# Performance work log

Hardware: AMD Instinct MI355X
Metric: run time of the kernel (lower is better)

## Reference

```python
import jax, jax.numpy as jnp
import numpy as np

N = 50000
E = 800000
D_IN, D_HID, D_OUT = 128, 128, 64


def setup_inputs() -> dict:
    key = jax.random.key(0)
    ks = jax.random.split(key, 8)
    x = jax.random.normal(ks[0], (N, D_IN), dtype=jnp.float32)
    edge_index = jax.random.randint(ks[1], (2, E), 0, N, dtype=jnp.int64)
    # Glorot-ish init for weights
    W1 = jax.random.normal(ks[2], (D_IN, D_HID), dtype=jnp.float32) / np.sqrt(D_IN)
    b1 = jnp.zeros((D_HID,), dtype=jnp.float32)
    W2 = jax.random.normal(ks[3], (D_HID, D_OUT), dtype=jnp.float32) / np.sqrt(D_HID)
    b2 = jnp.zeros((D_OUT,), dtype=jnp.float32)
    fc_W = jax.random.normal(ks[4], (D_OUT, D_OUT), dtype=jnp.float32) / np.sqrt(D_OUT)
    fc_b = jnp.zeros((D_OUT,), dtype=jnp.float32)
    return {"x": x, "edge_index": edge_index, "W1": W1, "b1": b1,
            "W2": W2, "b2": b2, "fc_W": fc_W, "fc_b": fc_b}


def _gcn_norm(edge_index, n_nodes):
    # PyG GCNConv default: add self-loops, symmetric normalization
    src, dst = edge_index[0], edge_index[1]
    loops = jnp.arange(n_nodes, dtype=edge_index.dtype)
    src = jnp.concatenate([src, loops])
    dst = jnp.concatenate([dst, loops])
    deg = jax.ops.segment_sum(jnp.ones_like(dst, dtype=jnp.float32), dst,
                              num_segments=n_nodes)
    dinv = jnp.where(deg > 0, jax.lax.rsqrt(deg), 0.0)
    norm = dinv[src] * dinv[dst]  # [E + N]
    return src, dst, norm


def _gcn_conv(x, src, dst, norm, W, b):
    h = x @ W                          # [N, d_out] transform first (fewer FLOPs)
    msg = h[src] * norm[:, None]       # gather + scale  [E+N, d_out]
    out = jax.ops.segment_sum(msg, dst, num_segments=x.shape[0])
    return out + b


def reference(x, edge_index, W1, b1, W2, b2, fc_W, fc_b):
    src, dst, norm = _gcn_norm(edge_index, x.shape[0])
    h = jax.nn.relu(_gcn_conv(x, src, dst, norm, W1, b1))
    h = jax.nn.relu(_gcn_conv(h, src, dst, norm, W2, b2))
    return h @ fc_W + fc_b
```

## Files before the change

kernel.cpp:

```cpp
#include <hip/hip_runtime.h>
#include <hip/hip_bf16.h>


typedef __attribute__((ext_vector_type(8))) short bf16x8;
typedef __attribute__((ext_vector_type(4))) float f32x4;

#define SLAB 64
#define BCAP 6144
#define BINCH 8192

__device__ __forceinline__ unsigned short f2bf(float f) {
    unsigned u = __float_as_uint(f);
    unsigned r = (u + 0x7FFFu + ((u >> 16) & 1u)) >> 16;
    return (unsigned short)r;
}
__device__ __forceinline__ float bf16_lo(unsigned u) {
    return __uint_as_float((u & 0xFFFFu) << 16);
}
__device__ __forceinline__ float bf16_hi(unsigned u) {
    return __uint_as_float(u & 0xFFFF0000u);
}


__global__ void k_wt(const float* __restrict__ W1, const float* __restrict__ W2,
                     const float* __restrict__ fcW,
                     unsigned short* __restrict__ W1T, unsigned short* __restrict__ W2T,
                     unsigned short* __restrict__ fcWT, int* __restrict__ gcnt,
                     unsigned short* __restrict__ hs1r, unsigned short* __restrict__ hs2,
                     float* __restrict__ dinv, int n) {
    int j = blockIdx.x * blockDim.x + threadIdx.x;
    if (j < 256) gcnt[j] = 0;
    if (j < 16384) {
        int m = j >> 7, k = j & 127;
        W1T[j] = f2bf(W1[k * 128 + m]);
    } else if (j < 24576) {
        int q = j - 16384;
        int m = q >> 7, k = q & 127;
        W2T[q] = f2bf(W2[k * 64 + m]);
    } else if (j < 28672) {
        int q = j - 24576;
        int m = q >> 6, k = q & 63;
        fcWT[q] = f2bf(fcW[k * 64 + m]);
    } else if (j < 28800) {
        hs1r[(size_t)n * 128 + (j - 28672)] = 0;
    } else if (j < 28864) {
        hs2[(size_t)n * 64 + (j - 28800)] = 0;
    } else if (j == 28864) {
        dinv[n] = 0.0f;
    }
}


__device__ __forceinline__ void gemm1_body(const float* __restrict__ X,
                                           const unsigned short* __restrict__ W1T,
                                           unsigned short* __restrict__ outp,
                                           int n, int blk, int tid,
                                           unsigned short* xs) {
    constexpr int LDW = 136;
    int base = blk * 64;
    for (int idx = tid; idx < 64 * 32; idx += 256) {
        int r = idx >> 5, c = idx & 31;
        int row = base + r;
        float4 v = make_float4(0.f, 0.f, 0.f, 0.f);
        if (row < n) v = ((const float4*)X)[(size_t)row * 32 + c];
        unsigned short* dp = &xs[r * LDW + c * 4];
        dp[0] = f2bf(v.x); dp[1] = f2bf(v.y); dp[2] = f2bf(v.z); dp[3] = f2bf(v.w);
    }
    __syncthreads();

    int wave = tid >> 6, lane = tid & 63;
    int quad = lane >> 4, l16 = lane & 15;
    int rbase = wave * 16;

    bf16x8 af[4];
#pragma unroll
    for (int kb = 0; kb < 4; ++kb)
        af[kb] = *(const bf16x8*)&xs[(rbase + l16) * LDW + kb * 32 + quad * 8];

#pragma unroll
    for (int jt = 0; jt < 8; ++jt) {
        f32x4 acc = {0.f, 0.f, 0.f, 0.f};
#pragma unroll
        for (int kb = 0; kb < 4; ++kb) {
            bf16x8 bf = *(const bf16x8*)&W1T[(size_t)(jt * 16 + l16) * 128 + kb * 32 + quad * 8];
            acc = __builtin_amdgcn_mfma_f32_16x16x32_bf16(af[kb], bf, acc, 0, 0, 0);
        }
#pragma unroll
        for (int r = 0; r < 4; ++r) {
            int row = base + rbase + quad * 4 + r;
            if (row < n)
                outp[(size_t)row * 128 + jt * 16 + l16] = f2bf(acc[r]);
        }
    }
}


__global__ __launch_bounds__(1024) void k_front(
    const int* __restrict__ src, const int* __restrict__ dst, int e,
    int* __restrict__ gcnt, unsigned* __restrict__ staging,
    const float* __restrict__ x, const unsigned short* __restrict__ W1T,
    unsigned short* __restrict__ hs1r, int n, int nbk, int ngemm) {
    __shared__ __align__(16) unsigned short xs4[4][64 * 136];
    __shared__ int bcnt[256], bpos[256], gofs[256];
    int bid = (int)blockIdx.x, tid = (int)threadIdx.x;

    if (bid < ngemm) {
        int tile = tid >> 8;
        gemm1_body(x, W1T, hs1r, n, bid * 4 + tile, tid & 255, xs4[tile]);
    } else {
        int b0 = bid - ngemm;
        if (tid < 256) { bcnt[tid] = 0; bpos[tid] = 0; }
        __syncthreads();
        int e0 = b0 * BINCH;
        int d[8], s[8];
#pragma unroll
        for (int r = 0; r < 8; ++r) {
            int i = e0 + r * 1024 + tid;
            if (i < e) { d[r] = dst[i]; s[r] = src[i]; } else d[r] = -1;
        }
#pragma unroll
        for (int r = 0; r < 8; ++r)
            if (d[r] >= 0) atomicAdd(&bcnt[d[r] >> 8], 1);
        __syncthreads();
        if (tid < nbk) {
            int c = bcnt[tid];
            gofs[tid] = c ? atomicAdd(&gcnt[tid], c) : 0;
        }
        __syncthreads();
#pragma unroll
        for (int r = 0; r < 8; ++r) {
            if (d[r] >= 0) {
                int b = d[r] >> 8;
                int p = atomicAdd(&bpos[b], 1);
                int idx = gofs[b] + p;
                if (idx < BCAP)
                    staging[(size_t)b * BCAP + idx] =
                        ((unsigned)d[r] << 16) | (unsigned)s[r];
            }
        }
    }
}


__global__ __launch_bounds__(1024) void k_scatter(
    const unsigned* __restrict__ staging, const int* __restrict__ gcnt,
    int* __restrict__ cnt, unsigned short* __restrict__ col,
    float* __restrict__ dinv, int n) {
    __shared__ int lcnt[256];
    __shared__ __align__(16) unsigned short ls[256 * SLAB];
    int b = (int)blockIdx.x, t = (int)threadIdx.x;
    if (t < 256) lcnt[t] = 0;
    unsigned sent2 = (unsigned)n | ((unsigned)n << 16);
    for (int i = t; i < 256 * SLAB / 2; i += 1024) ((unsigned*)ls)[i] = sent2;
    __syncthreads();
    int eb = gcnt[b]; if (eb > BCAP) eb = BCAP;
    const unsigned* sp = staging + (size_t)b * BCAP;
    for (int i = t; i < eb; i += 1024) {
        unsigned pk = sp[i];
        int dl = (int)(pk >> 16) & 255;
        int pos = atomicAdd(&lcnt[dl], 1);
        if (pos < SLAB) ls[(dl << 6) + pos] = (unsigned short)(pk & 0xFFFFu);
    }
    __syncthreads();
    int base = b << 8;
    const uint4* lsv = (const uint4*)ls;
    uint4* gv = (uint4*)(col + ((size_t)base << 6));
    for (int i = t; i < 256 * SLAB / 8; i += 1024) gv[i] = lsv[i];
    if (t < 256 && base + t < n) {
        int c = lcnt[t];
        cnt[base + t] = c;
        dinv[base + t] = rsqrtf((float)c + 1.0f);
    }
}


__global__ __launch_bounds__(256) void k_aggg128(
    const int* __restrict__ cnt, const unsigned short* __restrict__ col,
    const unsigned short* __restrict__ hs, const float* __restrict__ dinv,
    const float* __restrict__ bias, const unsigned short* __restrict__ W2T,
    unsigned short* __restrict__ hs2, int n) {
    __shared__ __align__(16) unsigned short ys[16 * 136];
    __shared__ float ldi[16];
    int tid = (int)threadIdx.x;
    int w = tid >> 6, lane = tid & 63;
    int half = lane >> 5, l32 = lane & 31;
    int gbase = (int)blockIdx.x * 16;
    const uint2* hp2 = (const uint2*)hs;

    for (int p = 0; p < 2; ++p) {
        int lrow = w * 4 + p * 2;
        int nodeA = gbase + lrow;
        int node = nodeA + half;
        int dA = cnt[nodeA], dB = cnt[nodeA + 1];
        if (dA > SLAB) dA = SLAB;
        if (dB > SLAB) dB = SLAB;
        int dmax = dA > dB ? dA : dB;
        const unsigned short* cp = &col[(size_t)node * SLAB];
        float di = dinv[node];
        uint2 su = hp2[(size_t)node * 32 + l32];
        float a0 = di * bf16_lo(su.x), a1 = di * bf16_hi(su.x);
        float a2 = di * bf16_lo(su.y), a3 = di * bf16_hi(su.y);
        float c0a = 0.f, c1a = 0.f, c2a = 0.f, c3a = 0.f;

        for (int i = 0; i < dmax; i += 16) {
            uint4 cA = *(const uint4*)&cp[i];
            uint4 cB = *(const uint4*)&cp[i + 8];
            int ci[16];
            ci[0] = cA.x & 0xFFFF; ci[1] = cA.x >> 16;
            ci[2] = cA.y & 0xFFFF; ci[3] = cA.y >> 16;
            ci[4] = cA.z & 0xFFFF; ci[5] = cA.z >> 16;
            ci[6] = cA.w & 0xFFFF; ci[7] = cA.w >> 16;
            ci[8] = cB.x & 0xFFFF; ci[9] = cB.x >> 16;
            ci[10] = cB.y & 0xFFFF; ci[11] = cB.y >> 16;
            ci[12] = cB.z & 0xFFFF; ci[13] = cB.z >> 16;
            ci[14] = cB.w & 0xFFFF; ci[15] = cB.w >> 16;
            uint2 u[16];
#pragma unroll
            for (int j = 0; j < 16; ++j) u[j] = hp2[(size_t)ci[j] * 32 + l32];
            float dw[16];
#pragma unroll
            for (int j = 0; j < 16; ++j) dw[j] = dinv[ci[j]];
#pragma unroll
            for (int j = 0; j < 16; j += 2) {
                a0 = fmaf(dw[j], bf16_lo(u[j].x), a0);
                a1 = fmaf(dw[j], bf16_hi(u[j].x), a1);
                a2 = fmaf(dw[j], bf16_lo(u[j].y), a2);
                a3 = fmaf(dw[j], bf16_hi(u[j].y), a3);
                c0a = fmaf(dw[j + 1], bf16_lo(u[j + 1].x), c0a);
                c1a = fmaf(dw[j + 1], bf16_hi(u[j + 1].x), c1a);
                c2a = fmaf(dw[j + 1], bf16_lo(u[j + 1].y), c2a);
                c3a = fmaf(dw[j + 1], bf16_hi(u[j + 1].y), c3a);
            }
        }
        float r0 = a0 + c0a, r1 = a1 + c1a, r2 = a2 + c2a, r3 = a3 + c3a;
        float4 bv = *(const float4*)&bias[l32 * 4];
        float v0 = fmaxf(di * r0 + bv.x, 0.0f);
        float v1 = fmaxf(di * r1 + bv.y, 0.0f);
        float v2 = fmaxf(di * r2 + bv.z, 0.0f);
        float v3 = fmaxf(di * r3 + bv.w, 0.0f);
        unsigned o0 = (unsigned)f2bf(v0) | ((unsigned)f2bf(v1) << 16);
        unsigned o1 = (unsigned)f2bf(v2) | ((unsigned)f2bf(v3) << 16);
        *(uint2*)((char*)ys + (size_t)(lrow + half) * 272 + l32 * 8) = make_uint2(o0, o1);
        if (l32 == 0) ldi[lrow + half] = di;
    }
    __syncthreads();

    int quad = lane >> 4, l16 = lane & 15;
    bf16x8 a[4];
#pragma unroll
    for (int kb = 0; kb < 4; ++kb)
        a[kb] = *(const bf16x8*)&ys[l16 * 136 + kb * 32 + quad * 8];
    f32x4 acc = {0.f, 0.f, 0.f, 0.f};
#pragma unroll
    for (int kb = 0; kb < 4; ++kb) {
        bf16x8 bf = *(const bf16x8*)&W2T[(size_t)(w * 16 + l16) * 128 + kb * 32 + quad * 8];
        acc = __builtin_amdgcn_mfma_f32_16x16x32_bf16(a[kb], bf, acc, 0, 0, 0);
    }
#pragma unroll
    for (int r = 0; r < 4; ++r) {
        int lrow = quad * 4 + r;
        int row = gbase + lrow;
        if (row < n)
            hs2[(size_t)row * 64 + w * 16 + l16] = f2bf(acc[r] * ldi[lrow]);
    }
}


__global__ __launch_bounds__(256) void k_aggg64(
    const int* __restrict__ cnt, const unsigned short* __restrict__ col,
    const unsigned short* __restrict__ hs, const float* __restrict__ dinv,
    const float* __restrict__ bias, const unsigned short* __restrict__ fcWT,
    const float* __restrict__ fcb, float* __restrict__ out, int n) {
    __shared__ __align__(16) unsigned short yt[16 * 72];
    int tid = (int)threadIdx.x;
    int w = tid >> 6, lane = tid & 63;
    int half = lane >> 5, l32 = lane & 31;
    int gbase = (int)blockIdx.x * 16;
    const unsigned* hp = (const unsigned*)hs;

    for (int p = 0; p < 2; ++p) {
        int lrow = w * 4 + p * 2;
        int nodeA = gbase + lrow;
        int node = nodeA + half;
        int dA = cnt[nodeA], dB = cnt[nodeA + 1];
        if (dA > SLAB) dA = SLAB;
        if (dB > SLAB) dB = SLAB;
        int dmax = dA > dB ? dA : dB;
        const unsigned short* cp = &col[(size_t)node * SLAB];
        float di = dinv[node];
        unsigned su = hp[(size_t)node * 32 + l32];
        float a0 = bf16_lo(su), a1 = bf16_hi(su);
        float b0 = 0.f, b1 = 0.f;

        for (int i = 0; i < dmax; i += 16) {
            uint4 cA = *(const uint4*)&cp[i];
            uint4 cB = *(const uint4*)&cp[i + 8];
            int ci[16];
            ci[0] = cA.x & 0xFFFF; ci[1] = cA.x >> 16;
            ci[2] = cA.y & 0xFFFF; ci[3] = cA.y >> 16;
            ci[4] = cA.z & 0xFFFF; ci[5] = cA.z >> 16;
            ci[6] = cA.w & 0xFFFF; ci[7] = cA.w >> 16;
            ci[8] = cB.x & 0xFFFF; ci[9] = cB.x >> 16;
            ci[10] = cB.y & 0xFFFF; ci[11] = cB.y >> 16;
            ci[12] = cB.z & 0xFFFF; ci[13] = cB.z >> 16;
            ci[14] = cB.w & 0xFFFF; ci[15] = cB.w >> 16;
            unsigned u[16];
#pragma unroll
            for (int j = 0; j < 16; ++j) u[j] = hp[(size_t)ci[j] * 32 + l32];
#pragma unroll
            for (int j = 0; j < 16; j += 2) {
                a0 += bf16_lo(u[j]);     a1 += bf16_hi(u[j]);
                b0 += bf16_lo(u[j + 1]); b1 += bf16_hi(u[j + 1]);
            }
        }
        float2 bv = *(const float2*)&bias[l32 * 2];
        float v0 = fmaxf(di * (a0 + b0) + bv.x, 0.0f);
        float v1 = fmaxf(di * (a1 + b1) + bv.y, 0.0f);
        *(unsigned*)((char*)yt + (size_t)(lrow + half) * 144 + l32 * 4) =
            (unsigned)f2bf(v0) | ((unsigned)f2bf(v1) << 16);
    }
    __syncthreads();

    int quad = lane >> 4, l16 = lane & 15;
    bf16x8 a[2];
#pragma unroll
    for (int kb = 0; kb < 2; ++kb)
        a[kb] = *(const bf16x8*)&yt[l16 * 72 + kb * 32 + quad * 8];
    f32x4 acc = {0.f, 0.f, 0.f, 0.f};
#pragma unroll
    for (int kb = 0; kb < 2; ++kb) {
        bf16x8 bf = *(const bf16x8*)&fcWT[(size_t)(w * 16 + l16) * 64 + kb * 32 + quad * 8];
        acc = __builtin_amdgcn_mfma_f32_16x16x32_bf16(a[kb], bf, acc, 0, 0, 0);
    }
    float bv = fcb[w * 16 + l16];
#pragma unroll
    for (int r = 0; r < 4; ++r) {
        int row = gbase + quad * 4 + r;
        if (row < n)
            out[(size_t)row * 64 + w * 16 + l16] = acc[r] + bv;
    }
}


extern "C" void kernel_launch(void* const* d_in, const int* in_sizes, int n_in,
                              void* d_out, int out_size, void* d_ws, size_t ws_size,
                              hipStream_t stream) {
    const float* x   = (const float*)d_in[0];
    const int*   ei  = (const int*)d_in[1];
    const float* W1  = (const float*)d_in[2];
    const float* b1  = (const float*)d_in[3];
    const float* W2  = (const float*)d_in[4];
    const float* b2  = (const float*)d_in[5];
    const float* fcW = (const float*)d_in[6];
    const float* fcb = (const float*)d_in[7];
    float* out = (float*)d_out;

    const int N = in_sizes[0] / 128;
    const int E = in_sizes[1] / 2;
    const int* src = ei;
    const int* dst = ei + E;

    const int NB    = (N + 255) >> 8;
    const int Npad  = NB << 8;
    const int nbin  = (E + BINCH - 1) / BINCH;
    const int gg64  = (N + 63) / 64;
    const int ngemm = (gg64 + 3) / 4;
    const int nagg  = (N + 15) / 16;

    auto align16 = [](size_t v) { return (v + 15) & ~(size_t)15; };
    char* p = (char*)d_ws;
    int* gcnt = (int*)p;                       p += align16(sizeof(int) * 256);
    unsigned* staging = (unsigned*)p;          p += align16(sizeof(unsigned) * (size_t)NB * BCAP);
    int* cnt = (int*)p;                        p += align16(sizeof(int) * N);
    float* dinv = (float*)p;                   p += align16(sizeof(float) * (N + 1));
    unsigned short* col = (unsigned short*)p;  p += align16(sizeof(unsigned short) * (size_t)Npad * SLAB);
    unsigned short* W1T = (unsigned short*)p;  p += align16(2 * 128 * 128);
    unsigned short* W2T = (unsigned short*)p;  p += align16(2 * 64 * 128);
    unsigned short* fcWT = (unsigned short*)p; p += align16(2 * 64 * 64);
    unsigned short* hs1r = (unsigned short*)p; p += align16(2 * ((size_t)N + 1) * 128);
    unsigned short* hs2 = (unsigned short*)p;  p += align16(2 * ((size_t)N + 1) * 64);

    k_wt<<<114, 256, 0, stream>>>(W1, W2, fcW, W1T, W2T, fcWT, gcnt,
                                  hs1r, hs2, dinv, N);

    k_front<<<ngemm + nbin, 1024, 0, stream>>>(src, dst, E, gcnt, staging,
                                               x, W1T, hs1r, N, NB, ngemm);
    k_scatter<<<NB, 1024, 0, stream>>>(staging, gcnt, cnt, col, dinv, N);

    k_aggg128<<<nagg, 256, 0, stream>>>(cnt, col, hs1r, dinv, b1, W2T, hs2, N);

    k_aggg64<<<nagg, 256, 0, stream>>>(cnt, col, hs2, dinv, b2, fcWT, fcb, out, N);
}
```

Before: 183.8 us.

## Prescale layer-1 features by dinv in scatter and process two nodes per wave

The scatter kernel now multiplies each node's layer-1 transformed features by its dinv in place, so the first aggregation no longer gathers dinv per neighbor and just sums pre-scaled rows. Both aggregation kernels are restructured so each half-wave handles two nodes at once with interleaved gathers, exposing more memory-level parallelism. The extra pass rewrites hs1 in place, costing additional read and write traffic and an extra bf16 rounding. cnt and dinv are padded to Npad so out-of-range nodes can be read safely.

```diff
diff --git a/kernel.cpp b/kernel.cpp
--- a/kernel.cpp
+++ b/kernel.cpp
@@ -20,6 +20,16 @@
 __device__ __forceinline__ float bf16_hi(unsigned u) {
     return __uint_as_float(u & 0xFFFF0000u);
 }
+
+#define UNPK16(cA, cB, ci)                                        \
+    ci[0] = cA.x & 0xFFFFu;  ci[1] = cA.x >> 16;                  \
+    ci[2] = cA.y & 0xFFFFu;  ci[3] = cA.y >> 16;                  \
+    ci[4] = cA.z & 0xFFFFu;  ci[5] = cA.z >> 16;                  \
+    ci[6] = cA.w & 0xFFFFu;  ci[7] = cA.w >> 16;                  \
+    ci[8] = cB.x & 0xFFFFu;  ci[9] = cB.x >> 16;                  \
+    ci[10] = cB.y & 0xFFFFu; ci[11] = cB.y >> 16;                 \
+    ci[12] = cB.z & 0xFFFFu; ci[13] = cB.z >> 16;                 \
+    ci[14] = cB.w & 0xFFFFu; ci[15] = cB.w >> 16;
 
 
 __global__ void k_wt(const float* __restrict__ W1, const float* __restrict__ W2,
@@ -27,7 +37,7 @@
                      unsigned short* __restrict__ W1T, unsigned short* __restrict__ W2T,
                      unsigned short* __restrict__ fcWT, int* __restrict__ gcnt,
                      unsigned short* __restrict__ hs1r, unsigned short* __restrict__ hs2,
-                     float* __restrict__ dinv, int n) {
+                     int n) {
     int j = blockIdx.x * blockDim.x + threadIdx.x;
     if (j < 256) gcnt[j] = 0;
     if (j < 16384) {
@@ -45,8 +55,6 @@
         hs1r[(size_t)n * 128 + (j - 28672)] = 0;
     } else if (j < 28864) {
         hs2[(size_t)n * 64 + (j - 28800)] = 0;
-    } else if (j == 28864) {
-        dinv[n] = 0.0f;
     }
 }
 
@@ -145,9 +153,10 @@
 __global__ __launch_bounds__(1024) void k_scatter(
     const unsigned* __restrict__ staging, const int* __restrict__ gcnt,
     int* __restrict__ cnt, unsigned short* __restrict__ col,
-    float* __restrict__ dinv, int n) {
+    float* __restrict__ dinv, unsigned* __restrict__ hs1u, int n) {
     __shared__ int lcnt[256];
     __shared__ __align__(16) unsigned short ls[256 * SLAB];
+    __shared__ float sdi[256];
     int b = (int)blockIdx.x, t = (int)threadIdx.x;
     if (t < 256) lcnt[t] = 0;
     unsigned sent2 = (unsigned)n | ((unsigned)n << 16);
@@ -166,10 +175,23 @@
     const uint4* lsv = (const uint4*)ls;
     uint4* gv = (uint4*)(col + ((size_t)base << 6));
     for (int i = t; i < 256 * SLAB / 8; i += 1024) gv[i] = lsv[i];
-    if (t < 256 && base + t < n) {
+    if (t < 256) {
         int c = lcnt[t];
+        float dv = rsqrtf((float)c + 1.0f);
+        sdi[t] = dv;
         cnt[base + t] = c;
-        dinv[base + t] = rsqrtf((float)c + 1.0f);
+        dinv[base + t] = dv;
+    }
+    __syncthreads();
+    int rows = n - base; if (rows > 256) rows = 256; if (rows < 0) rows = 0;
+    unsigned* hp = hs1u + ((size_t)base << 6);
+    for (int i = t; i < rows * 64; i += 1024) {
+        int r = i >> 6;
+        unsigned u = hp[i];
+        float sc = sdi[r];
+        unsigned lo = f2bf(sc * bf16_lo(u));
+        unsigned hi = f2bf(sc * bf16_hi(u));
+        hp[i] = lo | (hi << 16);
     }
 }
 
@@ -187,62 +209,65 @@
     int gbase = (int)blockIdx.x * 16;
     const uint2* hp2 = (const uint2*)hs;
 
-    for (int p = 0; p < 2; ++p) {
-        int lrow = w * 4 + p * 2;
-        int nodeA = gbase + lrow;
-        int node = nodeA + half;
-        int dA = cnt[nodeA], dB = cnt[nodeA + 1];
-        if (dA > SLAB) dA = SLAB;
-        if (dB > SLAB) dB = SLAB;
-        int dmax = dA > dB ? dA : dB;
-        const unsigned short* cp = &col[(size_t)node * SLAB];
-        float di = dinv[node];
-        uint2 su = hp2[(size_t)node * 32 + l32];
-        float a0 = di * bf16_lo(su.x), a1 = di * bf16_hi(su.x);
-        float a2 = di * bf16_lo(su.y), a3 = di * bf16_hi(su.y);
-        float c0a = 0.f, c1a = 0.f, c2a = 0.f, c3a = 0.f;
-
-        for (int i = 0; i < dmax; i += 16) {
-            uint4 cA = *(const uint4*)&cp[i];
-            uint4 cB = *(const uint4*)&cp[i + 8];
-            int ci[16];
-            ci[0] = cA.x & 0xFFFF; ci[1] = cA.x >> 16;
-            ci[2] = cA.y & 0xFFFF; ci[3] = cA.y >> 16;
-            ci[4] = cA.z & 0xFFFF; ci[5] = cA.z >> 16;
-            ci[6] = cA.w & 0xFFFF; ci[7] = cA.w >> 16;
-            ci[8] = cB.x & 0xFFFF; ci[9] = cB.x >> 16;
-            ci[10] = cB.y & 0xFFFF; ci[11] = cB.y >> 16;
-            ci[12] = cB.z & 0xFFFF; ci[13] = cB.z >> 16;
-            ci[14] = cB.w & 0xFFFF; ci[15] = cB.w >> 16;
-            uint2 u[16];
-#pragma unroll
-            for (int j = 0; j < 16; ++j) u[j] = hp2[(size_t)ci[j] * 32 + l32];
-            float dw[16];
-#pragma unroll
-            for (int j = 0; j < 16; ++j) dw[j] = dinv[ci[j]];
-#pragma unroll
-            for (int j = 0; j < 16; j += 2) {
-                a0 = fmaf(dw[j], bf16_lo(u[j].x), a0);
-                a1 = fmaf(dw[j], bf16_hi(u[j].x), a1);
-                a2 = fmaf(dw[j], bf16_lo(u[j].y), a2);
-                a3 = fmaf(dw[j], bf16_hi(u[j].y), a3);
-                c0a = fmaf(dw[j + 1], bf16_lo(u[j + 1].x), c0a);
-                c1a = fmaf(dw[j + 1], bf16_hi(u[j + 1].x), c1a);
-                c2a = fmaf(dw[j + 1], bf16_lo(u[j + 1].y), c2a);
-                c3a = fmaf(dw[j + 1], bf16_hi(u[j + 1].y), c3a);
-            }
-        }
-        float r0 = a0 + c0a, r1 = a1 + c1a, r2 = a2 + c2a, r3 = a3 + c3a;
-        float4 bv = *(const float4*)&bias[l32 * 4];
-        float v0 = fmaxf(di * r0 + bv.x, 0.0f);
-        float v1 = fmaxf(di * r1 + bv.y, 0.0f);
-        float v2 = fmaxf(di * r2 + bv.z, 0.0f);
-        float v3 = fmaxf(di * r3 + bv.w, 0.0f);
+    int n0 = gbase + w * 4 + half;
+    int n1 = n0 + 2;
+    int c0 = cnt[n0]; if (c0 > SLAB) c0 = SLAB;
+    int c1 = cnt[n1]; if (c1 > SLAB) c1 = SLAB;
+    int dm = c0 > c1 ? c0 : c1;
+    int dmo = __shfl_xor(dm, 32);
+    if (dmo > dm) dm = dmo;
+
+    const unsigned short* cp0 = &col[(size_t)n0 * SLAB];
+    const unsigned short* cp1 = &col[(size_t)n1 * SLAB];
+    float di0 = dinv[n0], di1 = dinv[n1];
+    int h0 = n0 < n ? n0 : n, h1 = n1 < n ? n1 : n;
+    uint2 s0 = hp2[(size_t)h0 * 32 + l32];
+    uint2 s1 = hp2[(size_t)h1 * 32 + l32];
+    float a0 = bf16_lo(s0.x), a1 = bf16_hi(s0.x), a2 = bf16_lo(s0.y), a3 = bf16_hi(s0.y);
+    float b0 = bf16_lo(s1.x), b1 = bf16_hi(s1.x), b2 = bf16_lo(s1.y), b3 = bf16_hi(s1.y);
+
+    for (int i = 0; i < dm; i += 16) {
+        uint4 cA0 = *(const uint4*)&cp0[i];
+        uint4 cB0 = *(const uint4*)&cp0[i + 8];
+        uint4 cA1 = *(const uint4*)&cp1[i];
+        uint4 cB1 = *(const uint4*)&cp1[i + 8];
+        unsigned ci0[16], ci1[16];
+        UNPK16(cA0, cB0, ci0)
+        UNPK16(cA1, cB1, ci1)
+        uint2 u0[16], u1[16];
+#pragma unroll
+        for (int j = 0; j < 16; ++j) u0[j] = hp2[(size_t)ci0[j] * 32 + l32];
+#pragma unroll
+        for (int j = 0; j < 16; ++j) u1[j] = hp2[(size_t)ci1[j] * 32 + l32];
+#pragma unroll
+        for (int j = 0; j < 16; ++j) {
+            a0 += bf16_lo(u0[j].x); a1 += bf16_hi(u0[j].x);
+            a2 += bf16_lo(u0[j].y); a3 += bf16_hi(u0[j].y);
+            b0 += bf16_lo(u1[j].x); b1 += bf16_hi(u1[j].x);
+            b2 += bf16_lo(u1[j].y); b3 += bf16_hi(u1[j].y);
+        }
+    }
+
+    float4 bv = *(const float4*)&bias[l32 * 4];
+    {
+        float v0 = fmaxf(di0 * a0 + bv.x, 0.0f);
+        float v1 = fmaxf(di0 * a1 + bv.y, 0.0f);
+        float v2 = fmaxf(di0 * a2 + bv.z, 0.0f);
+        float v3 = fmaxf(di0 * a3 + bv.w, 0.0f);
         unsigned o0 = (unsigned)f2bf(v0) | ((unsigned)f2bf(v1) << 16);
         unsigned o1 = (unsigned)f2bf(v2) | ((unsigned)f2bf(v3) << 16);
-        *(uint2*)((char*)ys + (size_t)(lrow + half) * 272 + l32 * 8) = make_uint2(o0, o1);
-        if (l32 == 0) ldi[lrow + half] = di;
-    }
+        *(uint2*)((char*)ys + (size_t)(w * 4 + half) * 272 + l32 * 8) = make_uint2(o0, o1);
+    }
+    {
+        float v0 = fmaxf(di1 * b0 + bv.x, 0.0f);
+        float v1 = fmaxf(di1 * b1 + bv.y, 0.0f);
+        float v2 = fmaxf(di1 * b2 + bv.z, 0.0f);
+        float v3 = fmaxf(di1 * b3 + bv.w, 0.0f);
+        unsigned o0 = (unsigned)f2bf(v0) | ((unsigned)f2bf(v1) << 16);
+        unsigned o1 = (unsigned)f2bf(v2) | ((unsigned)f2bf(v3) << 16);
+        *(uint2*)((char*)ys + (size_t)(w * 4 + 2 + half) * 272 + l32 * 8) = make_uint2(o0, o1);
+    }
+    if (l32 == 0) { ldi[w * 4 + half] = di0; ldi[w * 4 + 2 + half] = di1; }
     __syncthreads();
 
     int quad = lane >> 4, l16 = lane & 15;
@@ -278,45 +303,54 @@
     int gbase = (int)blockIdx.x * 16;
     const unsigned* hp = (const unsigned*)hs;
 
-    for (int p = 0; p < 2; ++p) {
-        int lrow = w * 4 + p * 2;
-        int nodeA = gbase + lrow;
-        int node = nodeA + half;
-        int dA = cnt[nodeA], dB = cnt[nodeA + 1];
-        if (dA > SLAB) dA = SLAB;
-        if (dB > SLAB) dB = SLAB;
-        int dmax = dA > dB ? dA : dB;
-        const unsigned short* cp = &col[(size_t)node * SLAB];
-        float di = dinv[node];
-        unsigned su = hp[(size_t)node * 32 + l32];
-        float a0 = bf16_lo(su), a1 = bf16_hi(su);
-        float b0 = 0.f, b1 = 0.f;
-
-        for (int i = 0; i < dmax; i += 16) {
-            uint4 cA = *(const uint4*)&cp[i];
-            uint4 cB = *(const uint4*)&cp[i + 8];
-            int ci[16];
-            ci[0] = cA.x & 0xFFFF; ci[1] = cA.x >> 16;
-            ci[2] = cA.y & 0xFFFF; ci[3] = cA.y >> 16;
-            ci[4] = cA.z & 0xFFFF; ci[5] = cA.z >> 16;
-            ci[6] = cA.w & 0xFFFF; ci[7] = cA.w >> 16;
-            ci[8] = cB.x & 0xFFFF; ci[9] = cB.x >> 16;
-            ci[10] = cB.y & 0xFFFF; ci[11] = cB.y >> 16;
-            ci[12] = cB.z & 0xFFFF; ci[13] = cB.z >> 16;
-            ci[14] = cB.w & 0xFFFF; ci[15] = cB.w >> 16;
-            unsigned u[16];
-#pragma unroll
-            for (int j = 0; j < 16; ++j) u[j] = hp[(size_t)ci[j] * 32 + l32];
-#pragma unroll
-            for (int j = 0; j < 16; j += 2) {
-                a0 += bf16_lo(u[j]);     a1 += bf16_hi(u[j]);
-                b0 += bf16_lo(u[j + 1]); b1 += bf16_hi(u[j + 1]);
-            }
-        }
-        float2 bv = *(const float2*)&bias[l32 * 2];
-        float v0 = fmaxf(di * (a0 + b0) + bv.x, 0.0f);
-        float v1 = fmaxf(di * (a1 + b1) + bv.y, 0.0f);
-        *(unsigned*)((char*)yt + (size_t)(lrow + half) * 144 + l32 * 4) =
+    int n0 = gbase + w * 4 + half;
+    int n1 = n0 + 2;
+    int c0 = cnt[n0]; if (c0 > SLAB) c0 = SLAB;
+    int c1 = cnt[n1]; if (c1 > SLAB) c1 = SLAB;
+    int dm = c0 > c1 ? c0 : c1;
+    int dmo = __shfl_xor(dm, 32);
+    if (dmo > dm) dm = dmo;
+
+    const unsigned short* cp0 = &col[(size_t)n0 * SLAB];
+    const unsigned short* cp1 = &col[(size_t)n1 * SLAB];
+    float di0 = dinv[n0], di1 = dinv[n1];
+    int h0 = n0 < n ? n0 : n, h1 = n1 < n ? n1 : n;
+    unsigned s0 = hp[(size_t)h0 * 32 + l32];
+    unsigned s1 = hp[(size_t)h1 * 32 + l32];
+    float a0 = bf16_lo(s0), a1 = bf16_hi(s0);
+    float b0 = bf16_lo(s1), b1 = bf16_hi(s1);
+
+    for (int i = 0; i < dm; i += 16) {
+        uint4 cA0 = *(const uint4*)&cp0[i];
+        uint4 cB0 = *(const uint4*)&cp0[i + 8];
+        uint4 cA1 = *(const uint4*)&cp1[i];
+        uint4 cB1 = *(const uint4*)&cp1[i + 8];
+        unsigned ci0[16], ci1[16];
+        UNPK16(cA0, cB0, ci0)
+        UNPK16(cA1, cB1, ci1)
+        unsigned u0[16], u1[16];
+#pragma unroll
+        for (int j = 0; j < 16; ++j) u0[j] = hp[(size_t)ci0[j] * 32 + l32];
+#pragma unroll
+        for (int j = 0; j < 16; ++j) u1[j] = hp[(size_t)ci1[j] * 32 + l32];
+#pragma unroll
+        for (int j = 0; j < 16; ++j) {
+            a0 += bf16_lo(u0[j]); a1 += bf16_hi(u0[j]);
+            b0 += bf16_lo(u1[j]); b1 += bf16_hi(u1[j]);
+        }
+    }
+
+    float2 bv = *(const float2*)&bias[l32 * 2];
+    {
+        float v0 = fmaxf(di0 * a0 + bv.x, 0.0f);
+        float v1 = fmaxf(di0 * a1 + bv.y, 0.0f);
+        *(unsigned*)((char*)yt + (size_t)(w * 4 + half) * 144 + l32 * 4) =
+            (unsigned)f2bf(v0) | ((unsigned)f2bf(v1) << 16);
+    }
+    {
+        float v0 = fmaxf(di1 * b0 + bv.x, 0.0f);
+        float v1 = fmaxf(di1 * b1 + bv.y, 0.0f);
+        *(unsigned*)((char*)yt + (size_t)(w * 4 + 2 + half) * 144 + l32 * 4) =
             (unsigned)f2bf(v0) | ((unsigned)f2bf(v1) << 16);
     }
     __syncthreads();
@@ -332,12 +366,12 @@
         bf16x8 bf = *(const bf16x8*)&fcWT[(size_t)(w * 16 + l16) * 64 + kb * 32 + quad * 8];
         acc = __builtin_amdgcn_mfma_f32_16x16x32_bf16(a[kb], bf, acc, 0, 0, 0);
     }
-    float bv = fcb[w * 16 + l16];
+    float bv2 = fcb[w * 16 + l16];
 #pragma unroll
     for (int r = 0; r < 4; ++r) {
         int row = gbase + quad * 4 + r;
         if (row < n)
-            out[(size_t)row * 64 + w * 16 + l16] = acc[r] + bv;
+            out[(size_t)row * 64 + w * 16 + l16] = acc[r] + bv2;
     }
 }
 
@@ -371,8 +405,8 @@
     char* p = (char*)d_ws;
     int* gcnt = (int*)p;                       p += align16(sizeof(int) * 256);
     unsigned* staging = (unsigned*)p;          p += align16(sizeof(unsigned) * (size_t)NB * BCAP);
-    int* cnt = (int*)p;                        p += align16(sizeof(int) * N);
-    float* dinv = (float*)p;                   p += align16(sizeof(float) * (N + 1));
+    int* cnt = (int*)p;                        p += align16(sizeof(int) * Npad);
+    float* dinv = (float*)p;                   p += align16(sizeof(float) * Npad);
     unsigned short* col = (unsigned short*)p;  p += align16(sizeof(unsigned short) * (size_t)Npad * SLAB);
     unsigned short* W1T = (unsigned short*)p;  p += align16(2 * 128 * 128);
     unsigned short* W2T = (unsigned short*)p;  p += align16(2 * 64 * 128);
@@ -381,11 +415,12 @@
     unsigned short* hs2 = (unsigned short*)p;  p += align16(2 * ((size_t)N + 1) * 64);
 
     k_wt<<<114, 256, 0, stream>>>(W1, W2, fcW, W1T, W2T, fcWT, gcnt,
-                                  hs1r, hs2, dinv, N);
+                                  hs1r, hs2, N);
 
     k_front<<<ngemm + nbin, 1024, 0, stream>>>(src, dst, E, gcnt, staging,
                                                x, W1T, hs1r, N, NB, ngemm);
-    k_scatter<<<NB, 1024, 0, stream>>>(staging, gcnt, cnt, col, dinv, N);
+    k_scatter<<<NB, 1024, 0, stream>>>(staging, gcnt, cnt, col, dinv,
+                                       (unsigned*)hs1r, N);
 
     k_aggg128<<<nagg, 256, 0, stream>>>(cnt, col, hs1r, dinv, b1, W2T, hs2, N);
 
```

After: 176.2 us. 1.04x faster.
